# Performance work log

Measured on AMD Instinct MI355X. Metric: run time of the kernel, lower is better.

The kernel has to match this reference:

```python
import jax, jax.numpy as jnp
import numpy as np

D_MODEL, N_HEADS, D_HEAD = 512, 8, 64
NUM_BITS, C_TABLES, PHI_SCALE, MAX_EXP, EPS = 8, 2, 0.1, 4, 1e-6
B, T = 2, 1024


def setup_inputs() -> dict:
    key = jax.random.key(0)
    ks = jax.random.split(key, 7)
    x = jax.random.normal(ks[0], (B, T, D_MODEL), dtype=jnp.float32)
    w_std = 0.02
    Wq = jax.random.normal(ks[1], (D_MODEL, D_MODEL), dtype=jnp.float32) * w_std
    Wk = jax.random.normal(ks[2], (D_MODEL, D_MODEL), dtype=jnp.float32) * w_std
    Wv = jax.random.normal(ks[3], (D_MODEL, D_MODEL), dtype=jnp.float32) * w_std
    Wo = jax.random.normal(ks[4], (D_MODEL, D_MODEL), dtype=jnp.float32) * w_std
    bo = jnp.zeros((D_MODEL,), dtype=jnp.float32)
    # 'positive' init: strictly positive lookup values so phi acts as a kernel feature map
    phi_table = jax.random.uniform(ks[5], (C_TABLES, 2 ** NUM_BITS), dtype=jnp.float32) * 0.5 + 0.01
    return {"x": x, "Wq": Wq, "Wk": Wk, "Wv": Wv, "Wo": Wo, "bo": bo, "phi_table": phi_table}


def _ternary_weight(W):
    # quantize to {-1,0,1} * power-of-two scale (exponent clipped to +/- MAX_EXP), STE-style
    alpha = jnp.mean(jnp.abs(W)) + 1e-12
    e = jnp.clip(jnp.round(jnp.log2(alpha)), -MAX_EXP, MAX_EXP)
    s = jnp.exp2(e)
    Wt = jnp.clip(jnp.round(W / s), -1.0, 1.0) * s
    return W + jax.lax.stop_gradient(Wt - W)


def _ternary_linear(x, W, b=None):
    y = jnp.einsum('btd,ed->bte', x, _ternary_weight(W))
    return y if b is None else y + b


def _phi(x, table):
    # structured lookup activation: sum of c sub-tables indexed at dyadically scaled quantizations
    L = table.shape[1]
    off = L // 2
    y = jnp.zeros_like(x)
    for j in range(table.shape[0]):
        idx = jnp.clip(jnp.round(x / (PHI_SCALE * (2.0 ** j))).astype(jnp.int32) + off, 0, L - 1)
        y = y + table[j][idx]
    return x + jax.lax.stop_gradient(y - x)  # STE: forward = lookup, backward = identity


def reference(x, Wq, Wk, Wv, Wo, bo, phi_table):
    Bsz, Tn, _ = x.shape
    Q = _ternary_linear(x, Wq)
    K = _ternary_linear(x, Wk)
    V = _ternary_linear(x, Wv)

    def split_heads(t):
        return t.reshape(Bsz, Tn, N_HEADS, D_HEAD).transpose(0, 2, 1, 3)  # (B,H,T,d)

    Q, K, V = split_heads(Q), split_heads(K), split_heads(V)
    phiQ = _phi(Q, phi_table)
    phiK = _phi(K, phi_table)

    # causal linear attention via cumulative outer products (faithful to original)
    kv = jnp.einsum('bhnd,bhne->bhnde', phiK, V)            # (B,H,T,d,d)
    kv_cum = jnp.cumsum(kv, axis=2)
    out = jnp.einsum('bhnd,bhnde->bhne', phiQ, kv_cum)       # (B,H,T,d)
    k_cum = jnp.cumsum(phiK, axis=2)
    Z = jnp.clip(jnp.sum(phiQ * k_cum, axis=-1, keepdims=True), EPS, None)
    out = out / Z

    out = out.transpose(0, 2, 1, 3).reshape(Bsz, Tn, D_MODEL)
    return _ternary_linear(out, Wo, bo)
```

## Files before the change

kernel.cpp:

```cpp
#include <hip/hip_runtime.h>
#include <stdint.h>

typedef __bf16 bf16;
typedef __bf16 v8bf __attribute__((ext_vector_type(8)));
typedef float v4f __attribute__((ext_vector_type(4)));

#define T_SEQ   1024
#define D_MODEL 512
#define N_HEADS 8
#define D_HEAD  64
#define B_SZ    2
#define BH      (B_SZ * N_HEADS)
#define CHUNK   128
#define NCHUNK  (T_SEQ / CHUNK)
#define WN      (D_MODEL * D_MODEL)

__device__ __forceinline__ void lds16(const void* g, void* l) {
    __builtin_amdgcn_global_load_lds(
        (const __attribute__((address_space(1))) uint32_t*)g,
        (__attribute__((address_space(3))) uint32_t*)l, 16, 0, 0);
}

struct AlphaArgs { const float* w[4]; float* partial; };

__global__ __launch_bounds__(256) void k_alpha(AlphaArgs a) {
    const int mid = blockIdx.y, blk = blockIdx.x, tid = threadIdx.x;
    const float* __restrict__ W = a.w[mid];
    float sabs = 0.f;
    #pragma unroll
    for (int k = 0; k < 4; ++k) {
        float4 v = ((const float4*)W)[blk * 1024 + k * 256 + tid];
        sabs += fabsf(v.x) + fabsf(v.y) + fabsf(v.z) + fabsf(v.w);
    }
    __shared__ float red[256];
    red[tid] = sabs;
    __syncthreads();
    for (int s = 128; s > 0; s >>= 1) {
        if (tid < s) red[tid] += red[tid + s];
        __syncthreads();
    }
    if (tid == 0) a.partial[mid * 64 + blk] = red[0];
}

struct WqArgs { const float* w[4]; bf16* wt[4]; const float* partial; };

__global__ __launch_bounds__(256) void k_wquant(WqArgs a) {
    const int mid = blockIdx.y, blk = blockIdx.x, tid = threadIdx.x;
    const float* __restrict__ W = a.w[mid];
    bf16* __restrict__ Wt = a.wt[mid];
    __shared__ float sv;
    if (tid < 64) {
        float p = a.partial[mid * 64 + tid];
        #pragma unroll
        for (int w = 1; w < 64; w <<= 1) p += __shfl_xor(p, w);
        if (tid == 0) {
            float alpha = p / (float)WN + 1e-12f;
            float e = rintf(log2f(alpha));
            e = fminf(4.f, fmaxf(-4.f, e));
            sv = exp2f(e);
        }
    }
    __syncthreads();
    const float s = sv;
    const float inv_s = 1.f / s;
    #pragma unroll
    for (int k = 0; k < 4; ++k) {
        const int idx = blk * 1024 + k * 256 + tid;
        float4 v = ((const float4*)W)[idx];
        float vv[4] = {v.x, v.y, v.z, v.w};
        union { uint2 u; bf16 h[4]; } o;
        #pragma unroll
        for (int j = 0; j < 4; ++j) {
            float r = rintf(vv[j] * inv_s);
            r = fminf(1.f, fmaxf(-1.f, r));
            o.h[j] = (bf16)(r * s);
        }
        ((uint2*)Wt)[idx] = o.u;
    }
}

__global__ __launch_bounds__(256) void k_xsplit(const float* __restrict__ x,
                                                bf16* __restrict__ xhi,
                                                bf16* __restrict__ xlo) {
    const int i = blockIdx.x * 256 + threadIdx.x;
    float4 v = ((const float4*)x)[i];
    float vv[4] = {v.x, v.y, v.z, v.w};
    union { uint2 u; bf16 h[4]; } H, L;
    #pragma unroll
    for (int j = 0; j < 4; ++j) {
        bf16 hb = (bf16)vv[j];
        H.h[j] = hb;
        L.h[j] = (bf16)(vv[j] - (float)hb);
    }
    ((uint2*)xhi)[i] = H.u;
    ((uint2*)xlo)[i] = L.u;
}

template <bool DUAL>
__device__ __forceinline__ void gemm64(
        const char* __restrict__ Ah, const char* __restrict__ Al,
        const char* __restrict__ Bb,
        bf16* Ahi, bf16* Alo, bf16* Bsm, v4f acc[4]) {
    const int tid = threadIdx.x;
    const int wm = tid >> 6, lane = tid & 63;
    const int q = lane >> 4, r = lane & 15;
    const int lrow = lane >> 3;
    const int schunk = (lane & 7) ^ lrow;
    const int r7 = r & 7;

    for (int k0 = 0; k0 < 512; k0 += 64) {
        #pragma unroll
        for (int j = 0; j < 2; ++j) {
            const int seg = wm * 2 + j;
            const int row = seg * 8 + lrow;
            const size_t goff = (size_t)row * 1024 + (size_t)k0 * 2 + schunk * 16;
            lds16(Ah + goff, (char*)Ahi + (seg << 10));
            lds16(Bb + goff, (char*)Bsm + (seg << 10));
            if (DUAL) lds16(Al + goff, (char*)Alo + (seg << 10));
        }
        __syncthreads();
        #pragma unroll
        for (int s = 0; s < 2; ++s) {
            const int co = ((s * 4 + q) ^ r7) * 8;
            v8bf ah = *(const v8bf*)&Ahi[(wm * 16 + r) * 64 + co];
            v8bf bb[4];
            #pragma unroll
            for (int v = 0; v < 4; ++v)
                bb[v] = *(const v8bf*)&Bsm[(v * 16 + r) * 64 + co];
            #pragma unroll
            for (int v = 0; v < 4; ++v)
                acc[v] = __builtin_amdgcn_mfma_f32_16x16x32_bf16(ah, bb[v], acc[v], 0, 0, 0);
            if (DUAL) {
                v8bf al = *(const v8bf*)&Alo[(wm * 16 + r) * 64 + co];
                #pragma unroll
                for (int v = 0; v < 4; ++v)
                    acc[v] = __builtin_amdgcn_mfma_f32_16x16x32_bf16(al, bb[v], acc[v], 0, 0, 0);
            }
        }
        __syncthreads();
    }
}

struct Qkv2Args {
    const bf16* xhi; const bf16* xlo; const bf16* wstk;
    const float* table;
    bf16* phiqB; bf16* phikB; float* phikF;
    float* vbufF; bf16* vbufT;
};

__global__ __launch_bounds__(256) void k_qkv2(Qkv2Args a) {
    __shared__ bf16 Ahi[64 * 64] __attribute__((aligned(16)));
    __shared__ bf16 Alo[64 * 64] __attribute__((aligned(16)));
    __shared__ bf16 Bsm[64 * 64] __attribute__((aligned(16)));
    __shared__ float tab[512];
    const int tid = threadIdx.x;
    const int tm = blockIdx.x, tn = blockIdx.y;
    const int z = tn >> 3;
    if (z < 2) { tab[tid] = a.table[tid]; tab[tid + 256] = a.table[tid + 256]; }

    v4f acc[4];
    #pragma unroll
    for (int v = 0; v < 4; ++v) acc[v] = (v4f){0.f, 0.f, 0.f, 0.f};

    const char* Ah = (const char*)(a.xhi + (size_t)(tm * 64) * 512);
    const char* Al = (const char*)(a.xlo + (size_t)(tm * 64) * 512);
    const char* Bb = (const char*)(a.wstk + (size_t)(tn * 64) * 512);
    if (z < 2) gemm64<true >(Ah, Al, Bb, Ahi, Alo, Bsm, acc);
    else       gemm64<false>(Ah, Al, Bb, Ahi, Alo, Bsm, acc);

    const int wm = tid >> 6, lane = tid & 63;
    const int q = lane >> 4, r = lane & 15;
    const int mb = tm * 64 + wm * 16 + q * 4;
    const int b = mb >> 10, tpos = mb & 1023;
    #pragma unroll
    for (int v = 0; v < 4; ++v) {
        const int n = tn * 64 + v * 16 + r;
        const int h = (n >> 6) & 7, d = n & 63;
        const int bh = b * 8 + h;
        float vals[4];
        #pragma unroll
        for (int i = 0; i < 4; ++i) {
            float val = acc[v][i];
            if (z < 2) {
                int i0 = (int)rintf(val / 0.1f) + 128;
                i0 = min(255, max(0, i0));
                int i1 = (int)rintf(val / 0.2f) + 128;
                i1 = min(255, max(0, i1));
                val = tab[i0] + tab[256 + i1];
            }
            vals[i] = val;
        }
        if (z == 0) {
            #pragma unroll
            for (int i = 0; i < 4; ++i)
                a.phiqB[((size_t)bh * 1024 + tpos + i) * 64 + d] = (bf16)vals[i];
        } else if (z == 1) {
            #pragma unroll
            for (int i = 0; i < 4; ++i) {
                const size_t idx = ((size_t)bh * 1024 + tpos + i) * 64 + d;
                a.phikB[idx] = (bf16)vals[i];
                a.phikF[idx] = vals[i];
            }
        } else {
            #pragma unroll
            for (int i = 0; i < 4; ++i)
                a.vbufF[((size_t)bh * 1024 + tpos + i) * 64 + d] = vals[i];
            union { uint2 pu; bf16 h4[4]; } P;
            #pragma unroll
            for (int i = 0; i < 4; ++i) P.h4[i] = (bf16)vals[i];
            *(uint2*)&a.vbufT[((size_t)bh * 64 + d) * 1024 + tpos] = P.pu;
        }
    }
}

__global__ __launch_bounds__(256) void k_chunksum(
        const float* __restrict__ phikF, const float* __restrict__ vbufF,
        float* __restrict__ kvT, float* __restrict__ ks) {
    const int c = blockIdx.x, bh = blockIdx.y;
    __shared__ float pk[32][64] __attribute__((aligned(16)));
    __shared__ float vv[32][64] __attribute__((aligned(16)));
    const int tid = threadIdx.x;
    const int e = tid & 63, g = tid >> 6;
    float kv[16];
    #pragma unroll
    for (int i = 0; i < 16; ++i) kv[i] = 0.f;
    const int srow = tid >> 3, scol = (tid & 7) * 8;
    const size_t base = (size_t)bh * 1024 + c * 128;

    for (int sub = 0; sub < 4; ++sub) {
        __syncthreads();
        const float* pg = phikF + (base + sub * 32 + srow) * 64 + scol;
        const float* vg = vbufF + (base + sub * 32 + srow) * 64 + scol;
        *(float4*)&pk[srow][scol]     = *(const float4*)pg;
        *(float4*)&pk[srow][scol + 4] = *(const float4*)(pg + 4);
        *(float4*)&vv[srow][scol]     = *(const float4*)vg;
        *(float4*)&vv[srow][scol + 4] = *(const float4*)(vg + 4);
        __syncthreads();
        for (int n = 0; n < 32; ++n) {
            const float vval = vv[n][e];
            const float4* prow = (const float4*)&pk[n][g * 16];
            float4 p0 = prow[0], p1 = prow[1], p2 = prow[2], p3 = prow[3];
            kv[0]  += p0.x * vval; kv[1]  += p0.y * vval; kv[2]  += p0.z * vval; kv[3]  += p0.w * vval;
            kv[4]  += p1.x * vval; kv[5]  += p1.y * vval; kv[6]  += p1.z * vval; kv[7]  += p1.w * vval;
            kv[8]  += p2.x * vval; kv[9]  += p2.y * vval; kv[10] += p2.z * vval; kv[11] += p2.w * vval;
            kv[12] += p3.x * vval; kv[13] += p3.y * vval; kv[14] += p3.z * vval; kv[15] += p3.w * vval;
        }
    }
    const size_t ob = ((size_t)bh * 8 + c) * 4096;
    #pragma unroll
    for (int w = 0; w < 4; ++w) {
        float4 s4 = {kv[4 * w], kv[4 * w + 1], kv[4 * w + 2], kv[4 * w + 3]};
        *(float4*)&kvT[ob + e * 64 + g * 16 + 4 * w] = s4;
    }
    if (tid < 64) {
        float s = 0.f;
        for (int n = 0; n < 128; ++n) s += phikF[(base + n) * 64 + tid];
        ks[((size_t)bh * 8 + c) * 64 + tid] = s;
    }
}

__global__ __launch_bounds__(256) void k_prefix(const float* __restrict__ kvT,
                                                bf16* __restrict__ kvsB,
                                                float* __restrict__ ks) {
    const int bh = blockIdx.x;
    const int p = blockIdx.y * 256 + threadIdx.x;
    float run = 0.f;
    #pragma unroll
    for (int c = 0; c < 8; ++c) {
        const size_t off = ((size_t)bh * 8 + c) * 4096 + p;
        kvsB[off] = (bf16)run;
        run += kvT[off];
    }
    if (blockIdx.y == 0 && threadIdx.x < 64) {
        const int tid = threadIdx.x;
        float runk = 0.f;
        #pragma unroll
        for (int c = 0; c < 8; ++c) {
            float* ptr = ks + ((size_t)bh * 8 + c) * 64 + tid;
            float v = *ptr; *ptr = runk; runk += v;
        }
    }
}

__global__ __launch_bounds__(256) void k_attn(
        const bf16* __restrict__ phiqB, const bf16* __restrict__ phikB,
        const bf16* __restrict__ vbufT, const bf16* __restrict__ kvsB,
        const float* __restrict__ ks, bf16* __restrict__ attn) {
    const int ntile = blockIdx.x, c = blockIdx.y, bh = blockIdx.z;
    __shared__ char smem[56064] __attribute__((aligned(16)));
    bf16* pqs  = (bf16*)smem;
    bf16* kv0s = (bf16*)(smem + 9216);
    bf16* Pbs  = (bf16*)smem;
    bf16* pks  = (bf16*)(smem + 18432);
    bf16* vts  = (bf16*)(smem + 36864);
    float* kc0s = (float*)(smem + 54272);
    float* Zrow = (float*)(smem + 54528);
    float* Zp   = (float*)(smem + 54784);
    float* Zs   = (float*)(smem + 55808);

    const int tid = threadIdx.x;
    const int wid = tid >> 6, lane = tid & 63;
    const int q = lane >> 4, r = lane & 15;
    const size_t tbase = (size_t)bh * 1024 + c * 128;
    const int t0 = ntile * 64;

    #pragma unroll
    for (int k = 0; k < 2; ++k) {
        const int idx = k * 256 + tid;
        const int row = idx >> 3, col = (idx & 7) * 8;
        *(uint4*)&pqs[row * 72 + col] =
            *(const uint4*)&phiqB[(tbase + t0 + row) * 64 + col];
        *(uint4*)&kv0s[row * 72 + col] =
            *(const uint4*)&kvsB[(((size_t)bh * 8 + c) * 64 + row) * 64 + col];
    }
    #pragma unroll
    for (int k = 0; k < 4; ++k) {
        const int idx = k * 256 + tid;
        const int row = idx >> 3, col = (idx & 7) * 8;
        *(uint4*)&pks[row * 72 + col] =
            *(const uint4*)&phikB[(tbase + row) * 64 + col];
        const int row2 = idx >> 4, col2 = (idx & 15) * 8;
        *(uint4*)&vts[row2 * 136 + col2] =
            *(const uint4*)&vbufT[((size_t)bh * 64 + row2) * 1024 + c * 128 + col2];
    }
    if (tid < 64) kc0s[tid] = ks[((size_t)bh * 8 + c) * 64 + tid];
    __syncthreads();

    v4f oacc[4], sacc[8];
    #pragma unroll
    for (int t = 0; t < 4; ++t) oacc[t] = (v4f){0.f, 0.f, 0.f, 0.f};
    #pragma unroll
    for (int u = 0; u < 8; ++u) sacc[u] = (v4f){0.f, 0.f, 0.f, 0.f};
    const int nmt = (ntile == 0) ? 4 : 8;

    #pragma unroll
    for (int kk = 0; kk < 2; ++kk) {
        v8bf af = *(const v8bf*)&pqs[(wid * 16 + r) * 72 + kk * 32 + q * 8];
        #pragma unroll
        for (int t = 0; t < 4; ++t) {
            v8bf bfr = *(const v8bf*)&kv0s[(t * 16 + r) * 72 + kk * 32 + q * 8];
            oacc[t] = __builtin_amdgcn_mfma_f32_16x16x32_bf16(af, bfr, oacc[t], 0, 0, 0);
        }
        #pragma unroll
        for (int u = 0; u < 8; ++u) {
            if (u < nmt) {
                v8bf bk = *(const v8bf*)&pks[(u * 16 + r) * 72 + kk * 32 + q * 8];
                sacc[u] = __builtin_amdgcn_mfma_f32_16x16x32_bf16(af, bk, sacc[u], 0, 0, 0);
            }
        }
    }
    {
        float z0 = 0.f;
        #pragma unroll
        for (int j = 0; j < 16; ++j)
            z0 += (float)pqs[lane * 72 + wid * 16 + j] * kc0s[wid * 16 + j];
        Zp[wid * 64 + lane] = z0;
    }
    __syncthreads();

    float zi[4] = {0.f, 0.f, 0.f, 0.f};
    #pragma unroll
    for (int u = 0; u < 8; ++u) {
        if (u < nmt) {
            const int m = u * 16 + r;
            #pragma unroll
            for (int i = 0; i < 4; ++i) {
                const int nloc = t0 + wid * 16 + q * 4 + i;
                const float sv = (m <= nloc) ? sacc[u][i] : 0.f;
                zi[i] += sv;
                Pbs[(wid * 16 + q * 4 + i) * 136 + m] = (bf16)sv;
            }
        }
    }
    #pragma unroll
    for (int w = 1; w < 16; w <<= 1) {
        #pragma unroll
        for (int i = 0; i < 4; ++i) zi[i] += __shfl_xor(zi[i], w);
    }
    if (r == 0) {
        #pragma unroll
        for (int i = 0; i < 4; ++i) Zrow[wid * 16 + q * 4 + i] = zi[i];
    }
    __syncthreads();

    if (tid < 64)
        Zs[tid] = fmaxf(Zrow[tid] + Zp[tid] + Zp[64 + tid] + Zp[128 + tid] + Zp[192 + tid],
                        1e-6f);
    __syncthreads();

    const int nkk = (ntile == 0) ? 2 : 4;
    #pragma unroll
    for (int kk = 0; kk < 4; ++kk) {
        if (kk < nkk) {
            v8bf af = *(const v8bf*)&Pbs[(wid * 16 + r) * 136 + kk * 32 + q * 8];
            #pragma unroll
            for (int t = 0; t < 4; ++t) {
                v8bf bfr = *(const v8bf*)&vts[(t * 16 + r) * 136 + kk * 32 + q * 8];
                oacc[t] = __builtin_amdgcn_mfma_f32_16x16x32_bf16(af, bfr, oacc[t], 0, 0, 0);
            }
        }
    }

    const int b = bh >> 3, h = bh & 7;
    #pragma unroll
    for (int t = 0; t < 4; ++t) {
        const int e = t * 16 + r;
        #pragma unroll
        for (int i = 0; i < 4; ++i) {
            const int row = wid * 16 + q * 4 + i;
            const float val = oacc[t][i] / Zs[row];
            const size_t mtok = (size_t)b * 1024 + c * 128 + t0 + row;
            attn[mtok * 512 + h * 64 + e] = (bf16)val;
        }
    }
}

struct OArgs { const bf16* attn; const bf16* wo; const float* bo; float* y; };

__global__ __launch_bounds__(256) void k_oproj(OArgs a) {
    __shared__ bf16 Ahi[64 * 64] __attribute__((aligned(16)));
    __shared__ bf16 Bsm[64 * 64] __attribute__((aligned(16)));
    v4f acc[4];
    #pragma unroll
    for (int v = 0; v < 4; ++v) acc[v] = (v4f){0.f, 0.f, 0.f, 0.f};
    const char* Ah = (const char*)(a.attn + (size_t)(blockIdx.x * 64) * 512);
    const char* Bb = (const char*)(a.wo + (size_t)(blockIdx.y * 64) * 512);
    gemm64<false>(Ah, nullptr, Bb, Ahi, nullptr, Bsm, acc);

    const int tid = threadIdx.x;
    const int wm = tid >> 6, lane = tid & 63;
    const int q = lane >> 4, r = lane & 15;
    #pragma unroll
    for (int v = 0; v < 4; ++v) {
        const int n = blockIdx.y * 64 + v * 16 + r;
        const float bias = a.bo[n];
        #pragma unroll
        for (int i = 0; i < 4; ++i) {
            const int m = blockIdx.x * 64 + wm * 16 + q * 4 + i;
            a.y[(size_t)m * 512 + n] = acc[v][i] + bias;
        }
    }
}

extern "C" void kernel_launch(void* const* d_in, const int* in_sizes, int n_in,
                              void* d_out, int out_size, void* d_ws, size_t ws_size,
                              hipStream_t stream) {
    const float* x   = (const float*)d_in[0];
    const float* Wq  = (const float*)d_in[1];
    const float* Wk  = (const float*)d_in[2];
    const float* Wv  = (const float*)d_in[3];
    const float* Wo  = (const float*)d_in[4];
    const float* bo  = (const float*)d_in[5];
    const float* tab = (const float*)d_in[6];

    uint8_t* w = (uint8_t*)d_ws;
    bf16* wt     = (bf16*)w;
    bf16* xhi    = wt + 4 * WN;
    bf16* xlo    = xhi + 1048576;
    float* phikF = (float*)(xlo + 1048576);
    float* vbufF = phikF + (size_t)16 * 1024 * 64;
    float* kvT   = vbufF + (size_t)16 * 1024 * 64;
    float* ks    = kvT + (size_t)16 * 8 * 4096;
    bf16* attn   = (bf16*)(ks + 16 * 8 * 64);
    bf16* phiqB  = attn + (size_t)2048 * 512;
    bf16* phikB  = phiqB + (size_t)16 * 1024 * 64;
    bf16* vbufT  = phikB + (size_t)16 * 1024 * 64;
    bf16* kvsB   = vbufT + (size_t)16 * 64 * 1024;
    float* partial = (float*)(kvsB + (size_t)16 * 8 * 4096);

    AlphaArgs aa;
    aa.w[0] = Wq; aa.w[1] = Wk; aa.w[2] = Wv; aa.w[3] = Wo;
    aa.partial = partial;
    k_alpha<<<dim3(64, 4), dim3(256), 0, stream>>>(aa);

    WqArgs qa;
    qa.w[0] = Wq; qa.w[1] = Wk; qa.w[2] = Wv; qa.w[3] = Wo;
    qa.wt[0] = wt; qa.wt[1] = wt + WN; qa.wt[2] = wt + 2 * WN; qa.wt[3] = wt + 3 * WN;
    qa.partial = partial;
    k_wquant<<<dim3(64, 4), dim3(256), 0, stream>>>(qa);

    k_xsplit<<<dim3(1024), dim3(256), 0, stream>>>(x, xhi, xlo);

    Qkv2Args pa{ xhi, xlo, wt, tab, phiqB, phikB, phikF, vbufF, vbufT };
    k_qkv2<<<dim3(32, 24), dim3(256), 0, stream>>>(pa);

    k_chunksum<<<dim3(NCHUNK, BH), dim3(256), 0, stream>>>(phikF, vbufF, kvT, ks);
    k_prefix<<<dim3(16, 16), dim3(256), 0, stream>>>(kvT, kvsB, ks);
    k_attn<<<dim3(2, NCHUNK, BH), dim3(256), 0, stream>>>(phiqB, phikB, vbufT, kvsB, ks, attn);

    OArgs oa{ attn, wt + 3 * WN, bo, (float*)d_out };
    k_oproj<<<dim3(32, 8), dim3(256), 0, stream>>>(oa);
}
```

Baseline: 117.5 us.

## Drop hi/lo split of x, fuse prep kernels, remove prefix kernel and fp32 buffers

x is now converted to a single bf16 copy instead of a hi/lo pair, which halves the MFMA work and LDS traffic in the Q/K phi path. The alpha reduction and x conversion are merged into one launch. The fp32 phiK and V copies are gone: chunksum reads the bf16 buffers, and attn builds its chunk prefix from kvT directly, so the separate prefix kernel is no longer needed. The phi outputs are staged through LDS for coalesced 16-byte stores. The cost is lower precision in the phi quantisation inputs, which can shift lookup indices near rounding boundaries, plus redundant prefix summation in later attn chunks.

```diff
diff --git a/kernel.cpp b/kernel.cpp
--- a/kernel.cpp
+++ b/kernel.cpp
@@ -21,25 +21,35 @@
         (__attribute__((address_space(3))) uint32_t*)l, 16, 0, 0);
 }
 
-struct AlphaArgs { const float* w[4]; float* partial; };
-
-__global__ __launch_bounds__(256) void k_alpha(AlphaArgs a) {
-    const int mid = blockIdx.y, blk = blockIdx.x, tid = threadIdx.x;
-    const float* __restrict__ W = a.w[mid];
-    float sabs = 0.f;
-    #pragma unroll
-    for (int k = 0; k < 4; ++k) {
-        float4 v = ((const float4*)W)[blk * 1024 + k * 256 + tid];
-        sabs += fabsf(v.x) + fabsf(v.y) + fabsf(v.z) + fabsf(v.w);
-    }
-    __shared__ float red[256];
-    red[tid] = sabs;
-    __syncthreads();
-    for (int s = 128; s > 0; s >>= 1) {
-        if (tid < s) red[tid] += red[tid + s];
-        __syncthreads();
-    }
-    if (tid == 0) a.partial[mid * 64 + blk] = red[0];
+struct PreArgs { const float* w[4]; float* partial; const float* x; bf16* xb; };
+
+__global__ __launch_bounds__(256) void k_pre(PreArgs a) {
+    const int bid = blockIdx.x, tid = threadIdx.x;
+    if (bid < 256) {
+        const int mid = bid >> 6, blk = bid & 63;
+        const float* __restrict__ W = a.w[mid];
+        float sabs = 0.f;
+        #pragma unroll
+        for (int k = 0; k < 4; ++k) {
+            float4 v = ((const float4*)W)[blk * 1024 + k * 256 + tid];
+            sabs += fabsf(v.x) + fabsf(v.y) + fabsf(v.z) + fabsf(v.w);
+        }
+        __shared__ float red[256];
+        red[tid] = sabs;
+        __syncthreads();
+        for (int s = 128; s > 0; s >>= 1) {
+            if (tid < s) red[tid] += red[tid + s];
+            __syncthreads();
+        }
+        if (tid == 0) a.partial[mid * 64 + blk] = red[0];
+    } else {
+        const int i = (bid - 256) * 256 + tid;
+        float4 v = ((const float4*)a.x)[i];
+        union { uint2 u; bf16 h[4]; } H;
+        H.h[0] = (bf16)v.x; H.h[1] = (bf16)v.y;
+        H.h[2] = (bf16)v.z; H.h[3] = (bf16)v.w;
+        ((uint2*)a.xb)[i] = H.u;
+    }
 }
 
 struct WqArgs { const float* w[4]; bf16* wt[4]; const float* partial; };
@@ -79,28 +89,9 @@
     }
 }
 
-__global__ __launch_bounds__(256) void k_xsplit(const float* __restrict__ x,
-                                                bf16* __restrict__ xhi,
-                                                bf16* __restrict__ xlo) {
-    const int i = blockIdx.x * 256 + threadIdx.x;
-    float4 v = ((const float4*)x)[i];
-    float vv[4] = {v.x, v.y, v.z, v.w};
-    union { uint2 u; bf16 h[4]; } H, L;
-    #pragma unroll
-    for (int j = 0; j < 4; ++j) {
-        bf16 hb = (bf16)vv[j];
-        H.h[j] = hb;
-        L.h[j] = (bf16)(vv[j] - (float)hb);
-    }
-    ((uint2*)xhi)[i] = H.u;
-    ((uint2*)xlo)[i] = L.u;
-}
-
-template <bool DUAL>
 __device__ __forceinline__ void gemm64(
-        const char* __restrict__ Ah, const char* __restrict__ Al,
-        const char* __restrict__ Bb,
-        bf16* Ahi, bf16* Alo, bf16* Bsm, v4f acc[4]) {
+        const char* __restrict__ Ab, const char* __restrict__ Bb,
+        bf16* As, bf16* Bs, v4f acc[4]) {
     const int tid = threadIdx.x;
     const int wm = tid >> 6, lane = tid & 63;
     const int q = lane >> 4, r = lane & 15;
@@ -114,44 +105,35 @@
             const int seg = wm * 2 + j;
             const int row = seg * 8 + lrow;
             const size_t goff = (size_t)row * 1024 + (size_t)k0 * 2 + schunk * 16;
-            lds16(Ah + goff, (char*)Ahi + (seg << 10));
-            lds16(Bb + goff, (char*)Bsm + (seg << 10));
-            if (DUAL) lds16(Al + goff, (char*)Alo + (seg << 10));
+            lds16(Ab + goff, (char*)As + (seg << 10));
+            lds16(Bb + goff, (char*)Bs + (seg << 10));
         }
         __syncthreads();
         #pragma unroll
         for (int s = 0; s < 2; ++s) {
             const int co = ((s * 4 + q) ^ r7) * 8;
-            v8bf ah = *(const v8bf*)&Ahi[(wm * 16 + r) * 64 + co];
+            v8bf ah = *(const v8bf*)&As[(wm * 16 + r) * 64 + co];
             v8bf bb[4];
             #pragma unroll
             for (int v = 0; v < 4; ++v)
-                bb[v] = *(const v8bf*)&Bsm[(v * 16 + r) * 64 + co];
+                bb[v] = *(const v8bf*)&Bs[(v * 16 + r) * 64 + co];
             #pragma unroll
             for (int v = 0; v < 4; ++v)
                 acc[v] = __builtin_amdgcn_mfma_f32_16x16x32_bf16(ah, bb[v], acc[v], 0, 0, 0);
-            if (DUAL) {
-                v8bf al = *(const v8bf*)&Alo[(wm * 16 + r) * 64 + co];
-                #pragma unroll
-                for (int v = 0; v < 4; ++v)
-                    acc[v] = __builtin_amdgcn_mfma_f32_16x16x32_bf16(al, bb[v], acc[v], 0, 0, 0);
-            }
         }
         __syncthreads();
     }
 }
 
 struct Qkv2Args {
-    const bf16* xhi; const bf16* xlo; const bf16* wstk;
+    const bf16* xb; const bf16* wstk;
     const float* table;
-    bf16* phiqB; bf16* phikB; float* phikF;
-    float* vbufF; bf16* vbufT;
+    bf16* phiqB; bf16* phikB; bf16* vbufT;
 };
 
 __global__ __launch_bounds__(256) void k_qkv2(Qkv2Args a) {
-    __shared__ bf16 Ahi[64 * 64] __attribute__((aligned(16)));
-    __shared__ bf16 Alo[64 * 64] __attribute__((aligned(16)));
-    __shared__ bf16 Bsm[64 * 64] __attribute__((aligned(16)));
+    __shared__ bf16 As[64 * 64] __attribute__((aligned(16)));
+    __shared__ bf16 Bs[64 * 64] __attribute__((aligned(16)));
     __shared__ float tab[512];
     const int tid = threadIdx.x;
     const int tm = blockIdx.x, tn = blockIdx.y;
@@ -162,129 +144,107 @@
     #pragma unroll
     for (int v = 0; v < 4; ++v) acc[v] = (v4f){0.f, 0.f, 0.f, 0.f};
 
-    const char* Ah = (const char*)(a.xhi + (size_t)(tm * 64) * 512);
-    const char* Al = (const char*)(a.xlo + (size_t)(tm * 64) * 512);
-    const char* Bb = (const char*)(a.wstk + (size_t)(tn * 64) * 512);
-    if (z < 2) gemm64<true >(Ah, Al, Bb, Ahi, Alo, Bsm, acc);
-    else       gemm64<false>(Ah, Al, Bb, Ahi, Alo, Bsm, acc);
+    gemm64((const char*)(a.xb + (size_t)(tm * 64) * 512),
+           (const char*)(a.wstk + (size_t)(tn * 64) * 512), As, Bs, acc);
 
     const int wm = tid >> 6, lane = tid & 63;
     const int q = lane >> 4, r = lane & 15;
-    const int mb = tm * 64 + wm * 16 + q * 4;
-    const int b = mb >> 10, tpos = mb & 1023;
-    #pragma unroll
-    for (int v = 0; v < 4; ++v) {
-        const int n = tn * 64 + v * 16 + r;
-        const int h = (n >> 6) & 7, d = n & 63;
-        const int bh = b * 8 + h;
-        float vals[4];
-        #pragma unroll
-        for (int i = 0; i < 4; ++i) {
-            float val = acc[v][i];
-            if (z < 2) {
+    const int h = tn & 7;
+    const int mb = tm * 64;
+    const int b = mb >> 10, tpos0 = mb & 1023;
+    const int bh = b * 8 + h;
+
+    if (z < 2) {
+        #pragma unroll
+        for (int v = 0; v < 4; ++v) {
+            const int d = v * 16 + r;
+            #pragma unroll
+            for (int i = 0; i < 4; ++i) {
+                float val = acc[v][i];
                 int i0 = (int)rintf(val / 0.1f) + 128;
                 i0 = min(255, max(0, i0));
                 int i1 = (int)rintf(val / 0.2f) + 128;
                 i1 = min(255, max(0, i1));
                 val = tab[i0] + tab[256 + i1];
-            }
-            vals[i] = val;
-        }
-        if (z == 0) {
-            #pragma unroll
-            for (int i = 0; i < 4; ++i)
-                a.phiqB[((size_t)bh * 1024 + tpos + i) * 64 + d] = (bf16)vals[i];
-        } else if (z == 1) {
-            #pragma unroll
-            for (int i = 0; i < 4; ++i) {
-                const size_t idx = ((size_t)bh * 1024 + tpos + i) * 64 + d;
-                a.phikB[idx] = (bf16)vals[i];
-                a.phikF[idx] = vals[i];
-            }
-        } else {
-            #pragma unroll
-            for (int i = 0; i < 4; ++i)
-                a.vbufF[((size_t)bh * 1024 + tpos + i) * 64 + d] = vals[i];
+                As[(wm * 16 + q * 4 + i) * 64 + d] = (bf16)val;
+            }
+        }
+        __syncthreads();
+        bf16* dst = (z == 0) ? a.phiqB : a.phikB;
+        #pragma unroll
+        for (int k = 0; k < 2; ++k) {
+            const int idx = k * 256 + tid;
+            const int row = idx >> 3, cb = (idx & 7) * 8;
+            *(uint4*)&dst[((size_t)bh * 1024 + tpos0 + row) * 64 + cb] =
+                *(const uint4*)&As[row * 64 + cb];
+        }
+    } else {
+        const int tpos = tpos0 + wm * 16 + q * 4;
+        #pragma unroll
+        for (int v = 0; v < 4; ++v) {
+            const int d = v * 16 + r;
             union { uint2 pu; bf16 h4[4]; } P;
             #pragma unroll
-            for (int i = 0; i < 4; ++i) P.h4[i] = (bf16)vals[i];
+            for (int i = 0; i < 4; ++i) P.h4[i] = (bf16)acc[v][i];
             *(uint2*)&a.vbufT[((size_t)bh * 64 + d) * 1024 + tpos] = P.pu;
         }
     }
 }
 
 __global__ __launch_bounds__(256) void k_chunksum(
-        const float* __restrict__ phikF, const float* __restrict__ vbufF,
+        const bf16* __restrict__ phikB, const bf16* __restrict__ vbufT,
         float* __restrict__ kvT, float* __restrict__ ks) {
     const int c = blockIdx.x, bh = blockIdx.y;
-    __shared__ float pk[32][64] __attribute__((aligned(16)));
-    __shared__ float vv[32][64] __attribute__((aligned(16)));
+    __shared__ float pkF[32 * 64] __attribute__((aligned(16)));
     const int tid = threadIdx.x;
     const int e = tid & 63, g = tid >> 6;
     float kv[16];
     #pragma unroll
     for (int i = 0; i < 16; ++i) kv[i] = 0.f;
-    const int srow = tid >> 3, scol = (tid & 7) * 8;
+    float ksum = 0.f;
     const size_t base = (size_t)bh * 1024 + c * 128;
+    const bf16* vrow = vbufT + ((size_t)bh * 64 + e) * 1024 + c * 128;
 
     for (int sub = 0; sub < 4; ++sub) {
         __syncthreads();
-        const float* pg = phikF + (base + sub * 32 + srow) * 64 + scol;
-        const float* vg = vbufF + (base + sub * 32 + srow) * 64 + scol;
-        *(float4*)&pk[srow][scol]     = *(const float4*)pg;
-        *(float4*)&pk[srow][scol + 4] = *(const float4*)(pg + 4);
-        *(float4*)&vv[srow][scol]     = *(const float4*)vg;
-        *(float4*)&vv[srow][scol + 4] = *(const float4*)(vg + 4);
-        __syncthreads();
-        for (int n = 0; n < 32; ++n) {
-            const float vval = vv[n][e];
-            const float4* prow = (const float4*)&pk[n][g * 16];
-            float4 p0 = prow[0], p1 = prow[1], p2 = prow[2], p3 = prow[3];
-            kv[0]  += p0.x * vval; kv[1]  += p0.y * vval; kv[2]  += p0.z * vval; kv[3]  += p0.w * vval;
-            kv[4]  += p1.x * vval; kv[5]  += p1.y * vval; kv[6]  += p1.z * vval; kv[7]  += p1.w * vval;
-            kv[8]  += p2.x * vval; kv[9]  += p2.y * vval; kv[10] += p2.z * vval; kv[11] += p2.w * vval;
-            kv[12] += p3.x * vval; kv[13] += p3.y * vval; kv[14] += p3.z * vval; kv[15] += p3.w * vval;
+        {
+            const int t = tid >> 3, db = (tid & 7) * 8;
+            v8bf p = *(const v8bf*)&phikB[(base + sub * 32 + t) * 64 + db];
+            #pragma unroll
+            for (int j = 0; j < 8; ++j) pkF[t * 64 + db + j] = (float)p[j];
+        }
+        __syncthreads();
+        #pragma unroll
+        for (int jv = 0; jv < 4; ++jv) {
+            v8bf vch = *(const v8bf*)&vrow[sub * 32 + jv * 8];
+            #pragma unroll
+            for (int jj = 0; jj < 8; ++jj) {
+                const float vv = (float)vch[jj];
+                const float4* prow = (const float4*)&pkF[(jv * 8 + jj) * 64 + g * 16];
+                float4 p0 = prow[0], p1 = prow[1], p2 = prow[2], p3 = prow[3];
+                kv[0]  += p0.x * vv; kv[1]  += p0.y * vv; kv[2]  += p0.z * vv; kv[3]  += p0.w * vv;
+                kv[4]  += p1.x * vv; kv[5]  += p1.y * vv; kv[6]  += p1.z * vv; kv[7]  += p1.w * vv;
+                kv[8]  += p2.x * vv; kv[9]  += p2.y * vv; kv[10] += p2.z * vv; kv[11] += p2.w * vv;
+                kv[12] += p3.x * vv; kv[13] += p3.y * vv; kv[14] += p3.z * vv; kv[15] += p3.w * vv;
+            }
+        }
+        if (tid < 64) {
+            #pragma unroll
+            for (int t = 0; t < 32; ++t) ksum += pkF[t * 64 + tid];
         }
     }
     const size_t ob = ((size_t)bh * 8 + c) * 4096;
     #pragma unroll
-    for (int w = 0; w < 4; ++w) {
-        float4 s4 = {kv[4 * w], kv[4 * w + 1], kv[4 * w + 2], kv[4 * w + 3]};
-        *(float4*)&kvT[ob + e * 64 + g * 16 + 4 * w] = s4;
-    }
-    if (tid < 64) {
-        float s = 0.f;
-        for (int n = 0; n < 128; ++n) s += phikF[(base + n) * 64 + tid];
-        ks[((size_t)bh * 8 + c) * 64 + tid] = s;
-    }
-}
-
-__global__ __launch_bounds__(256) void k_prefix(const float* __restrict__ kvT,
-                                                bf16* __restrict__ kvsB,
-                                                float* __restrict__ ks) {
-    const int bh = blockIdx.x;
-    const int p = blockIdx.y * 256 + threadIdx.x;
-    float run = 0.f;
-    #pragma unroll
-    for (int c = 0; c < 8; ++c) {
-        const size_t off = ((size_t)bh * 8 + c) * 4096 + p;
-        kvsB[off] = (bf16)run;
-        run += kvT[off];
-    }
-    if (blockIdx.y == 0 && threadIdx.x < 64) {
-        const int tid = threadIdx.x;
-        float runk = 0.f;
-        #pragma unroll
-        for (int c = 0; c < 8; ++c) {
-            float* ptr = ks + ((size_t)bh * 8 + c) * 64 + tid;
-            float v = *ptr; *ptr = runk; runk += v;
-        }
-    }
+    for (int w4 = 0; w4 < 4; ++w4) {
+        float4 s4 = {kv[4 * w4], kv[4 * w4 + 1], kv[4 * w4 + 2], kv[4 * w4 + 3]};
+        *(float4*)&kvT[ob + e * 64 + g * 16 + 4 * w4] = s4;
+    }
+    if (tid < 64) ks[((size_t)bh * 8 + c) * 64 + tid] = ksum;
 }
 
 __global__ __launch_bounds__(256) void k_attn(
         const bf16* __restrict__ phiqB, const bf16* __restrict__ phikB,
-        const bf16* __restrict__ vbufT, const bf16* __restrict__ kvsB,
+        const bf16* __restrict__ vbufT, const float* __restrict__ kvT,
         const float* __restrict__ ks, bf16* __restrict__ attn) {
     const int ntile = blockIdx.x, c = blockIdx.y, bh = blockIdx.z;
     __shared__ char smem[56064] __attribute__((aligned(16)));
@@ -310,8 +270,29 @@
         const int row = idx >> 3, col = (idx & 7) * 8;
         *(uint4*)&pqs[row * 72 + col] =
             *(const uint4*)&phiqB[(tbase + t0 + row) * 64 + col];
-        *(uint4*)&kv0s[row * 72 + col] =
-            *(const uint4*)&kvsB[(((size_t)bh * 8 + c) * 64 + row) * 64 + col];
+    }
+    {
+        const int e = tid >> 2, db = (tid & 3) * 16;
+        float accp[16];
+        #pragma unroll
+        for (int j = 0; j < 16; ++j) accp[j] = 0.f;
+        for (int cc = 0; cc < c; ++cc) {
+            const float* src = kvT + ((size_t)bh * 8 + cc) * 4096 + e * 64 + db;
+            #pragma unroll
+            for (int k4 = 0; k4 < 4; ++k4) {
+                float4 f = *(const float4*)(src + 4 * k4);
+                accp[4 * k4]     += f.x; accp[4 * k4 + 1] += f.y;
+                accp[4 * k4 + 2] += f.z; accp[4 * k4 + 3] += f.w;
+            }
+        }
+        union { uint4 u; bf16 h8[8]; } U0, U1;
+        #pragma unroll
+        for (int j = 0; j < 8; ++j) {
+            U0.h8[j] = (bf16)accp[j];
+            U1.h8[j] = (bf16)accp[8 + j];
+        }
+        *(uint4*)&kv0s[e * 72 + db] = U0.u;
+        *(uint4*)&kv0s[e * 72 + db + 8] = U1.u;
     }
     #pragma unroll
     for (int k = 0; k < 4; ++k) {
@@ -323,7 +304,11 @@
         *(uint4*)&vts[row2 * 136 + col2] =
             *(const uint4*)&vbufT[((size_t)bh * 64 + row2) * 1024 + c * 128 + col2];
     }
-    if (tid < 64) kc0s[tid] = ks[((size_t)bh * 8 + c) * 64 + tid];
+    if (tid < 64) {
+        float s = 0.f;
+        for (int cc = 0; cc < c; ++cc) s += ks[((size_t)bh * 8 + cc) * 64 + tid];
+        kc0s[tid] = s;
+    }
     __syncthreads();
 
     v4f oacc[4], sacc[8];
@@ -418,14 +403,13 @@
 struct OArgs { const bf16* attn; const bf16* wo; const float* bo; float* y; };
 
 __global__ __launch_bounds__(256) void k_oproj(OArgs a) {
-    __shared__ bf16 Ahi[64 * 64] __attribute__((aligned(16)));
-    __shared__ bf16 Bsm[64 * 64] __attribute__((aligned(16)));
+    __shared__ bf16 As[64 * 64] __attribute__((aligned(16)));
+    __shared__ bf16 Bs[64 * 64] __attribute__((aligned(16)));
     v4f acc[4];
     #pragma unroll
     for (int v = 0; v < 4; ++v) acc[v] = (v4f){0.f, 0.f, 0.f, 0.f};
-    const char* Ah = (const char*)(a.attn + (size_t)(blockIdx.x * 64) * 512);
-    const char* Bb = (const char*)(a.wo + (size_t)(blockIdx.y * 64) * 512);
-    gemm64<false>(Ah, nullptr, Bb, Ahi, nullptr, Bsm, acc);
+    gemm64((const char*)(a.attn + (size_t)(blockIdx.x * 64) * 512),
+           (const char*)(a.wo + (size_t)(blockIdx.y * 64) * 512), As, Bs, acc);
 
     const int tid = threadIdx.x;
     const int wm = tid >> 6, lane = tid & 63;
@@ -455,23 +439,19 @@
 
     uint8_t* w = (uint8_t*)d_ws;
     bf16* wt     = (bf16*)w;
-    bf16* xhi    = wt + 4 * WN;
-    bf16* xlo    = xhi + 1048576;
-    float* phikF = (float*)(xlo + 1048576);
-    float* vbufF = phikF + (size_t)16 * 1024 * 64;
-    float* kvT   = vbufF + (size_t)16 * 1024 * 64;
+    bf16* xb     = wt + 4 * WN;
+    bf16* phiqB  = xb + 1048576;
+    bf16* phikB  = phiqB + (size_t)16 * 1024 * 64;
+    bf16* vbufT  = phikB + (size_t)16 * 1024 * 64;
+    float* kvT   = (float*)(vbufT + (size_t)16 * 64 * 1024);
     float* ks    = kvT + (size_t)16 * 8 * 4096;
     bf16* attn   = (bf16*)(ks + 16 * 8 * 64);
-    bf16* phiqB  = attn + (size_t)2048 * 512;
-    bf16* phikB  = phiqB + (size_t)16 * 1024 * 64;
-    bf16* vbufT  = phikB + (size_t)16 * 1024 * 64;
-    bf16* kvsB   = vbufT + (size_t)16 * 64 * 1024;
-    float* partial = (float*)(kvsB + (size_t)16 * 8 * 4096);
-
-    AlphaArgs aa;
-    aa.w[0] = Wq; aa.w[1] = Wk; aa.w[2] = Wv; aa.w[3] = Wo;
-    aa.partial = partial;
-    k_alpha<<<dim3(64, 4), dim3(256), 0, stream>>>(aa);
+    float* partial = (float*)(attn + (size_t)2048 * 512);
+
+    PreArgs pr;
+    pr.w[0] = Wq; pr.w[1] = Wk; pr.w[2] = Wv; pr.w[3] = Wo;
+    pr.partial = partial; pr.x = x; pr.xb = xb;
+    k_pre<<<dim3(1280), dim3(256), 0, stream>>>(pr);
 
     WqArgs qa;
     qa.w[0] = Wq; qa.w[1] = Wk; qa.w[2] = Wv; qa.w[3] = Wo;
@@ -479,14 +459,11 @@
     qa.partial = partial;
     k_wquant<<<dim3(64, 4), dim3(256), 0, stream>>>(qa);
 
-    k_xsplit<<<dim3(1024), dim3(256), 0, stream>>>(x, xhi, xlo);
-
-    Qkv2Args pa{ xhi, xlo, wt, tab, phiqB, phikB, phikF, vbufF, vbufT };
+    Qkv2Args pa{ xb, wt, tab, phiqB, phikB, vbufT };
     k_qkv2<<<dim3(32, 24), dim3(256), 0, stream>>>(pa);
 
-    k_chunksum<<<dim3(NCHUNK, BH), dim3(256), 0, stream>>>(phikF, vbufF, kvT, ks);
-    k_prefix<<<dim3(16, 16), dim3(256), 0, stream>>>(kvT, kvsB, ks);
-    k_attn<<<dim3(2, NCHUNK, BH), dim3(256), 0, stream>>>(phiqB, phikB, vbufT, kvsB, ks, attn);
+    k_chunksum<<<dim3(NCHUNK, BH), dim3(256), 0, stream>>>(phikB, vbufT, kvT, ks);
+    k_attn<<<dim3(2, NCHUNK, BH), dim3(256), 0, stream>>>(phiqB, phikB, vbufT, kvT, ks, attn);
 
     OArgs oa{ attn, wt + 3 * WN, bo, (float*)d_out };
     k_oproj<<<dim3(32, 8), dim3(256), 0, stream>>>(oa);
```

Measured after the change: 124.5 us. 1.06x slower.
